# Performance work log

Hardware: AMD Instinct MI355X
Metric: run time of the kernel (lower is better)

Reference implementation:

```python
import jax, jax.numpy as jnp
import numpy as np

B, N, D, H = 4, 4096, 1024, 16
DH = D // H            # 64
GH = 4 * DH            # gate hidden = 256
FREQ = N // 2 + 1      # 2049
INV_SQRT2 = 0.7071067811865476


def _ln(x, g, b, eps=1e-6):
    mu = jnp.mean(x, axis=-1, keepdims=True)
    var = jnp.mean((x - mu) ** 2, axis=-1, keepdims=True)
    return (x - mu) / jnp.sqrt(var + eps) * g + b


def _xavier(k, out_f, in_f, gain=0.8):
    bound = gain * (6.0 / (in_f + out_f)) ** 0.5
    return jax.random.uniform(k, (out_f, in_f), jnp.float32, -bound, bound)


def setup_inputs() -> dict:
    key = jax.random.key(0)
    ks = jax.random.split(key, 8)
    return {
        'x': jax.random.normal(ks[0], (B, N, D), jnp.float32),
        'Wq': _xavier(ks[1], D, D),
        'Wv': _xavier(ks[2], D, D),
        'Wo': _xavier(ks[3], D, D),
        'ln_g': jnp.ones((DH,), jnp.float32),
        'ln_b': jnp.zeros((DH,), jnp.float32),
        'Wgup': _xavier(ks[4], GH, DH),
        'Wgdn': _xavier(ks[5], 2 * FREQ, GH),
        'Wwup': _xavier(ks[6], GH, DH),
        'Wwdn': _xavier(ks[7], N, GH),
    }


def reference(x, Wq, Wv, Wo, ln_g, ln_b, Wgup, Wgdn, Wwup, Wwdn):
    Bx, Nx, Dx = x.shape
    # projections -> [B, H, N, DH]
    q = (x @ Wq.T).reshape(Bx, Nx, H, DH).transpose(0, 2, 1, 3)
    v = (x @ Wv.T).reshape(Bx, Nx, H, DH).transpose(0, 2, 1, 3)
    # per-head summary token -> complex spectral gate over FREQ bins
    bar = _ln(q.mean(axis=2), ln_g, ln_b)                    # [B, H, DH]
    gr = (jax.nn.silu(bar @ Wgup.T) @ Wgdn.T)               # [B, H, 2*FREQ]
    gr = gr.reshape(Bx, H, FREQ, 2)
    gate = jax.lax.complex(gr[..., 0], gr[..., 1])           # [B, H, FREQ]
    # spectral mixing (chunk == seq_len, power-of-two path)
    spec = jnp.fft.rfft(v, axis=2, norm='ortho') * gate[..., None]
    v_t = jnp.fft.irfft(spec, n=Nx, axis=2, norm='ortho')    # [B, H, N, DH]
    # Haar wavelet refinement
    even, odd = v_t[..., ::2, :], v_t[..., 1::2, :]
    w = jnp.concatenate([even + odd, even - odd], axis=-2) * INV_SQRT2
    s = (jax.nn.silu(bar @ Wwup.T) @ Wwdn.T)[..., None]      # [B, H, N, 1]
    w = w * s
    half = Nx // 2
    low, high = w[..., :half, :], w[..., half:, :]
    # interleave even/odd back along seq dim
    refine = jnp.stack([low + high, low - high], axis=-2).reshape(Bx, H, Nx, DH) * INV_SQRT2
    v_t = v_t + refine
    y = v_t.transpose(0, 2, 1, 3).reshape(Bx, Nx, Dx)
    return y @ Wo.T
```

## Files before the change

### kernel.cpp

```cpp
#include <hip/hip_runtime.h>

constexpr int CB = 4, CN = 4096, CD = 1024, CH = 16, CDH = 64, CGH = 256, CFREQ = 2049, CBH = 64;

constexpr size_t OFF_XSUM = 0;
constexpr size_t OFF_HG   = 4096;
constexpr size_t OFF_HW   = OFF_HG + (size_t)CBH * CGH;
constexpr size_t OFF_GATE = OFF_HW + (size_t)CBH * CGH;
constexpr size_t OFF_S    = OFF_GATE + (size_t)CBH * 2 * CFREQ;
constexpr size_t OFF_CA   = OFF_S + (size_t)CBH * CN;
constexpr size_t OFF_CD   = OFF_CA + (size_t)CBH * (CN / 2);
constexpr size_t OFF_TW   = OFF_CD + (size_t)CBH * (CN / 2);
constexpr size_t OFF_VCOL = OFF_TW + 8192;
constexpr size_t OFF_XHI  = OFF_VCOL + (size_t)CB * CD * CN;
constexpr size_t OFF_XLO  = OFF_XHI + (size_t)CB * CN * CD / 2;
constexpr size_t OFF_WVHI = OFF_XLO + (size_t)CB * CN * CD / 2;
constexpr size_t OFF_WVLO = OFF_WVHI + (size_t)CD * CD / 2;
constexpr size_t OFF_WOHI = OFF_WVLO + (size_t)CD * CD / 2;
constexpr size_t OFF_WOLO = OFF_WOHI + (size_t)CD * CD / 2;

typedef __bf16 bf16x8 __attribute__((ext_vector_type(8)));
typedef __bf16 bf16x4 __attribute__((ext_vector_type(4)));
typedef float  f32x4  __attribute__((ext_vector_type(4)));

__device__ __forceinline__ float silu_f(float x) { return x / (1.0f + expf(-x)); }

__device__ __forceinline__ void gload16(const void* g, void* l) {
    __builtin_amdgcn_global_load_lds(
        reinterpret_cast<const __attribute__((address_space(1))) unsigned int*>(
            reinterpret_cast<uintptr_t>(g)),
        reinterpret_cast<__attribute__((address_space(3))) unsigned int*>(
            reinterpret_cast<uintptr_t>(l)),
        16, 0, 0);
}

__device__ __forceinline__ float2 cadd(float2 a, float2 b) { return make_float2(a.x + b.x, a.y + b.y); }
__device__ __forceinline__ float2 csub(float2 a, float2 b) { return make_float2(a.x - b.x, a.y - b.y); }
__device__ __forceinline__ float2 cmul(float2 a, float2 b) { return make_float2(a.x * b.x - a.y * b.y, a.x * b.y + a.y * b.x); }
__device__ __forceinline__ float2 cmulc(float2 a, float2 b) { return make_float2(a.x * b.x + a.y * b.y, a.y * b.x - a.x * b.y); }
__device__ __forceinline__ float2 mulni(float2 a) { return make_float2(a.y, -a.x); }
__device__ __forceinline__ float2 mulpi(float2 a) { return make_float2(-a.y, a.x); }

__device__ __forceinline__ int P(int r) { return r + (r >> 3); }

__device__ __forceinline__ int drev8(int k) {
    return ((k & 7) << 9) | (((k >> 3) & 7) << 6) | (((k >> 6) & 7) << 3) | ((k >> 9) & 7);
}

__device__ __forceinline__ void dft8_fwd(const float2 a[8], float2 A[8]) {
    float2 t0 = cadd(a[0], a[4]), t1 = csub(a[0], a[4]);
    float2 t2 = cadd(a[2], a[6]), t3 = mulni(csub(a[2], a[6]));
    float2 t4 = cadd(a[1], a[5]), t5 = csub(a[1], a[5]);
    float2 t6 = cadd(a[3], a[7]), t7 = mulni(csub(a[3], a[7]));
    float2 u0 = cadd(t0, t2), u1 = csub(t0, t2);
    float2 u2 = cadd(t1, t3), u3 = csub(t1, t3);
    float2 u4 = cadd(t4, t6), u5 = mulni(csub(t4, t6));
    float2 u6 = cadd(t5, t7), u7 = csub(t5, t7);
    const float s = 0.70710678118654752f;
    float2 w6 = make_float2(s * (u6.x + u6.y), s * (u6.y - u6.x));
    float2 w7 = make_float2(s * (u7.y - u7.x), -s * (u7.x + u7.y));
    A[0] = cadd(u0, u4); A[4] = csub(u0, u4);
    A[2] = cadd(u1, u5); A[6] = csub(u1, u5);
    A[1] = cadd(u2, w6); A[5] = csub(u2, w6);
    A[3] = cadd(u3, w7); A[7] = csub(u3, w7);
}

__device__ __forceinline__ void dft8_inv(const float2 a[8], float2 A[8]) {
    float2 t0 = cadd(a[0], a[4]), t1 = csub(a[0], a[4]);
    float2 t2 = cadd(a[2], a[6]), t3 = mulpi(csub(a[2], a[6]));
    float2 t4 = cadd(a[1], a[5]), t5 = csub(a[1], a[5]);
    float2 t6 = cadd(a[3], a[7]), t7 = mulpi(csub(a[3], a[7]));
    float2 u0 = cadd(t0, t2), u1 = csub(t0, t2);
    float2 u2 = cadd(t1, t3), u3 = csub(t1, t3);
    float2 u4 = cadd(t4, t6), u5 = mulpi(csub(t4, t6));
    float2 u6 = cadd(t5, t7), u7 = csub(t5, t7);
    const float s = 0.70710678118654752f;
    float2 w6 = make_float2(s * (u6.x - u6.y), s * (u6.x + u6.y));
    float2 w7 = make_float2(-s * (u7.x + u7.y), s * (u7.x - u7.y));
    A[0] = cadd(u0, u4); A[4] = csub(u0, u4);
    A[2] = cadd(u1, u5); A[6] = csub(u1, u5);
    A[1] = cadd(u2, w6); A[5] = csub(u2, w6);
    A[3] = cadd(u3, w7); A[7] = csub(u3, w7);
}

template <int M>
__device__ __forceinline__ void fwd_stage(float2* buf, const float2* __restrict__ tw, int t) {
    int j = t & (M - 1);
    int i0 = ((t & ~(M - 1)) << 3) + j;
    constexpr int TS = 512 / M;
    float2 a[8], A[8];
#pragma unroll
    for (int c = 0; c < 8; ++c) a[c] = buf[P(i0 + c * M)];
    dft8_fwd(a, A);
#pragma unroll
    for (int p = 0; p < 8; ++p) {
        float2 v = (M > 1 && p) ? cmul(A[p], tw[j * p * TS]) : A[p];
        buf[P(i0 + p * M)] = v;
    }
}

template <int M>
__device__ __forceinline__ void inv_stage(float2* buf, const float2* __restrict__ tw, int t) {
    int j = t & (M - 1);
    int i0 = ((t & ~(M - 1)) << 3) + j;
    constexpr int TS = 512 / M;
    float2 a[8], A[8];
#pragma unroll
    for (int c = 0; c < 8; ++c) {
        float2 v = buf[P(i0 + c * M)];
        a[c] = (M > 1 && c) ? cmulc(v, tw[j * c * TS]) : v;
    }
    dft8_inv(a, A);
#pragma unroll
    for (int p = 0; p < 8; ++p) buf[P(i0 + p * M)] = A[p];
}

__global__ void k_tw(float* twf) {
    int i = blockIdx.x * 256 + threadIdx.x;
    if (i < 4096) {
        double ang = -2.0 * 3.14159265358979323846 * (double)i / 4096.0;
        twf[2 * i]     = (float)cos(ang);
        twf[2 * i + 1] = (float)sin(ang);
    }
}

__global__ __launch_bounds__(256) void k_meansplit(const float* __restrict__ X, float* __restrict__ xsum,
                                                   __bf16* __restrict__ hi, __bf16* __restrict__ lo) {
    int b = blockIdx.y;
    int c = blockIdx.x;
    int t = threadIdx.x;
    int half = t >> 7;
    int col = (t & 127) * 8;
    size_t base = (size_t)b * CN * CD + ((size_t)c * 64 + half * 32) * CD + col;
    float acc[8];
#pragma unroll
    for (int j = 0; j < 8; ++j) acc[j] = 0.f;
    for (int n = 0; n < 32; ++n) {
        size_t o = base + (size_t)n * CD;
        float4 v0 = *(const float4*)(X + o);
        float4 v1 = *(const float4*)(X + o + 4);
        float vv[8] = {v0.x, v0.y, v0.z, v0.w, v1.x, v1.y, v1.z, v1.w};
        bf16x8 hv, lv;
#pragma unroll
        for (int j = 0; j < 8; ++j) {
            acc[j] += vv[j];
            __bf16 h = (__bf16)vv[j];
            hv[j] = h;
            lv[j] = (__bf16)(vv[j] - (float)h);
        }
        *(bf16x8*)&hi[o] = hv;
        *(bf16x8*)&lo[o] = lv;
    }
#pragma unroll
    for (int j = 0; j < 8; ++j) atomicAdd(&xsum[b * CD + col + j], acc[j]);
}

__global__ __launch_bounds__(256) void k_barhidden(const float* __restrict__ xsum,
                                                   const float* __restrict__ Wq,
                                                   const float* __restrict__ ln_g,
                                                   const float* __restrict__ ln_b,
                                                   const float* __restrict__ Wgup,
                                                   const float* __restrict__ Wwup,
                                                   float* __restrict__ hg, float* __restrict__ hw) {
    int bh = blockIdx.x;
    int b = bh >> 4, h = bh & 15;
    int t = threadIdx.x;
    __shared__ float part[256];
    __shared__ float bar_s[64];
    int dh = t >> 2, seg = t & 3;
    const float* wrow = Wq + (size_t)(h * 64 + dh) * CD + seg * 256;
    const float* xs = xsum + b * CD + seg * 256;
    float acc = 0.f;
    for (int i = 0; i < 256; i += 4) {
        float4 w4 = *(const float4*)(wrow + i);
        float4 x4 = *(const float4*)(xs + i);
        acc += w4.x * x4.x + w4.y * x4.y + w4.z * x4.z + w4.w * x4.w;
    }
    part[t] = acc;
    __syncthreads();
    if (t < 64) {
        float q = (part[4 * t] + part[4 * t + 1] + part[4 * t + 2] + part[4 * t + 3]) * (1.0f / 4096.0f);
        float mu = q;
        for (int o = 32; o >= 1; o >>= 1) mu += __shfl_xor(mu, o, 64);
        mu *= (1.0f / 64.0f);
        float dev = q - mu;
        float vv = dev * dev;
        for (int o = 32; o >= 1; o >>= 1) vv += __shfl_xor(vv, o, 64);
        vv *= (1.0f / 64.0f);
        bar_s[t] = dev / sqrtf(vv + 1e-6f) * ln_g[t] + ln_b[t];
    }
    __syncthreads();
    const float* gup = Wgup + (size_t)t * CDH;
    const float* wup = Wwup + (size_t)t * CDH;
    float ag = 0.f, aw = 0.f;
    for (int i = 0; i < CDH; i += 4) {
        float4 bb = *(const float4*)(&bar_s[i]);
        float4 g4 = *(const float4*)(gup + i);
        float4 w4 = *(const float4*)(wup + i);
        ag += g4.x * bb.x + g4.y * bb.y + g4.z * bb.z + g4.w * bb.w;
        aw += w4.x * bb.x + w4.y * bb.y + w4.z * bb.z + w4.w * bb.w;
    }
    hg[bh * CGH + t] = silu_f(ag);
    hw[bh * CGH + t] = silu_f(aw);
}

__global__ __launch_bounds__(256) void k_gategemv(const float* __restrict__ Wgdn,
                                                  const float* __restrict__ Wwdn,
                                                  const float* __restrict__ hg,
                                                  const float* __restrict__ hw,
                                                  float* __restrict__ gate, float* __restrict__ sbuf) {
    int z = blockIdx.z;
    const float* Wd = z ? Wwdn : Wgdn;
    const float* hid = z ? hw : hg;
    float* out = z ? sbuf : gate;
    int Kout = z ? CN : 2 * CFREQ;
    int bh0 = blockIdx.y * 8;
    int t = threadIdx.x;
    int k = blockIdx.x * 256 + t;
    __shared__ float Lh[8][256];
    for (int g = 0; g < 8; ++g) Lh[g][t] = hid[(size_t)(bh0 + g) * CGH + t];
    __syncthreads();
    if (k >= Kout) return;
    float accv[8] = {0.f, 0.f, 0.f, 0.f, 0.f, 0.f, 0.f, 0.f};
    const float* wrow = Wd + (size_t)k * CGH;
    for (int j4 = 0; j4 < 64; ++j4) {
        float4 wv = *(const float4*)(wrow + 4 * j4);
#pragma unroll
        for (int g = 0; g < 8; ++g) {
            accv[g] += wv.x * Lh[g][4 * j4] + wv.y * Lh[g][4 * j4 + 1] +
                       wv.z * Lh[g][4 * j4 + 2] + wv.w * Lh[g][4 * j4 + 3];
        }
    }
    for (int g = 0; g < 8; ++g) out[(size_t)(bh0 + g) * Kout + k] = accv[g];
}

__global__ __launch_bounds__(256) void k_coef(const float* __restrict__ sbuf,
                                              float* __restrict__ ca, float* __restrict__ cd) {
    int bh = blockIdx.y;
    int i = blockIdx.x * 256 + threadIdx.x;
    float s0 = sbuf[(size_t)bh * CN + i];
    float s1 = sbuf[(size_t)bh * CN + 2048 + i];
    ca[(size_t)bh * 2048 + i] = 1.0f + 0.5f * (s0 + s1);
    cd[(size_t)bh * 2048 + i] = 0.5f * (s0 - s1);
}

__global__ __launch_bounds__(256) void k_split(const float* __restrict__ src,
                                               __bf16* __restrict__ hi, __bf16* __restrict__ lo,
                                               int n4) {
    int i = blockIdx.x * 256 + threadIdx.x;
    int stride = gridDim.x * 256;
    for (; i < n4; i += stride) {
        float4 v = ((const float4*)src)[i];
        __bf16 h0 = (__bf16)v.x, h1 = (__bf16)v.y, h2 = (__bf16)v.z, h3 = (__bf16)v.w;
        bf16x4 hv = {h0, h1, h2, h3};
        bf16x4 lv = {(__bf16)(v.x - (float)h0), (__bf16)(v.y - (float)h1),
                     (__bf16)(v.z - (float)h2), (__bf16)(v.w - (float)h3)};
        *(bf16x4*)&hi[4 * (size_t)i] = hv;
        *(bf16x4*)&lo[4 * (size_t)i] = lv;
    }
}

__global__ __launch_bounds__(256) void k_tsplit(const float* __restrict__ Vcol,
                                                __bf16* __restrict__ hi, __bf16* __restrict__ lo) {
    __shared__ float tile[32][33];
    int bx = blockIdx.x;
    int by = blockIdx.y;
    int b  = blockIdx.z;
    int t = threadIdx.x;
    int d = t >> 3, n4 = (t & 7) * 4;
    const float* src = Vcol + ((size_t)b * CD + by * 32 + d) * CN + bx * 32 + n4;
    float4 v = *(const float4*)src;
    tile[d][n4] = v.x; tile[d][n4 + 1] = v.y; tile[d][n4 + 2] = v.z; tile[d][n4 + 3] = v.w;
    __syncthreads();
    int n = t >> 3, d4 = (t & 7) * 4;
    size_t o = ((size_t)b * CN + bx * 32 + n) * CD + by * 32 + d4;
    float x0 = tile[d4][n], x1 = tile[d4 + 1][n], x2 = tile[d4 + 2][n], x3 = tile[d4 + 3][n];
    __bf16 h0 = (__bf16)x0, h1 = (__bf16)x1, h2 = (__bf16)x2, h3 = (__bf16)x3;
    bf16x4 hv = {h0, h1, h2, h3};
    bf16x4 lv = {(__bf16)(x0 - (float)h0), (__bf16)(x1 - (float)h1),
                 (__bf16)(x2 - (float)h2), (__bf16)(x3 - (float)h3)};
    *(bf16x4*)&hi[o] = hv;
    *(bf16x4*)&lo[o] = lv;
}

template <int TRANS>
__global__ __launch_bounds__(256) void k_mfma_gemm(const __bf16* __restrict__ Ahi,
                                                   const __bf16* __restrict__ Alo,
                                                   const __bf16* __restrict__ Bhi,
                                                   const __bf16* __restrict__ Blo,
                                                   float* __restrict__ C) {
    __shared__ __align__(16) __bf16 lds[2][4][128 * 32];
    int t = threadIdx.x;
    int l = t & 63, w = t >> 6;
    int hw = blockIdx.x + (blockIdx.y << 3);
    int xcd = hw & 7, slot = hw >> 3;
    int m0 = (xcd * 16 + (slot >> 3)) * 128;
    int n0 = (slot & 7) * 128;
    int wm = w >> 1, wn = w & 1;

    const __bf16* gsrc = (w == 0) ? Ahi : (w == 1) ? Alo : (w == 2) ? Bhi : Blo;
    int gr0 = (w < 2) ? m0 : n0;
    unsigned o[8];
#pragma unroll
    for (int i = 0; i < 8; ++i) {
        int row = i * 16 + (l >> 2);
        unsigned slotq = (unsigned)((l & 3) ^ ((row >> 2) & 3));
        o[i] = (unsigned)(gr0 + row) * 1024u + slotq * 8u;
    }

    f32x4 acc[4][4];
#pragma unroll
    for (int m = 0; m < 4; ++m)
#pragma unroll
        for (int n = 0; n < 4; ++n) acc[m][n] = (f32x4){0.f, 0.f, 0.f, 0.f};

#pragma unroll
    for (int i = 0; i < 8; ++i)
        gload16(gsrc + (size_t)o[i], &lds[0][w][i * 512]);
    __syncthreads();

    int cur = 0;
#pragma unroll 2
    for (int k0 = 0; k0 < 1024; k0 += 32) {
        if (k0 + 32 < 1024) {
#pragma unroll
            for (int i = 0; i < 8; ++i)
                gload16(gsrc + ((size_t)o[i] + k0 + 32), &lds[cur ^ 1][w][i * 512]);
        }

        bf16x8 ah[4], al[4], bh[4], bl[4];
#pragma unroll
        for (int m = 0; m < 4; ++m) {
            int row = wm * 64 + m * 16 + (l & 15);
            int sl = (l >> 4) ^ ((row >> 2) & 3);
            ah[m] = *(const bf16x8*)&lds[cur][0][row * 32 + sl * 8];
            al[m] = *(const bf16x8*)&lds[cur][1][row * 32 + sl * 8];
        }
#pragma unroll
        for (int n = 0; n < 4; ++n) {
            int row = wn * 64 + n * 16 + (l & 15);
            int sl = (l >> 4) ^ ((row >> 2) & 3);
            bh[n] = *(const bf16x8*)&lds[cur][2][row * 32 + sl * 8];
            bl[n] = *(const bf16x8*)&lds[cur][3][row * 32 + sl * 8];
        }
#pragma unroll
        for (int m = 0; m < 4; ++m)
#pragma unroll
            for (int n = 0; n < 4; ++n) {
                acc[m][n] = __builtin_amdgcn_mfma_f32_16x16x32_bf16(ah[m], bh[n], acc[m][n], 0, 0, 0);
                acc[m][n] = __builtin_amdgcn_mfma_f32_16x16x32_bf16(ah[m], bl[n], acc[m][n], 0, 0, 0);
                acc[m][n] = __builtin_amdgcn_mfma_f32_16x16x32_bf16(al[m], bh[n], acc[m][n], 0, 0, 0);
            }
        __syncthreads();
        cur ^= 1;
    }

    if (TRANS) {
        int b = m0 >> 12;
        int tokb = (m0 & 4095) + wm * 64;
#pragma unroll
        for (int m = 0; m < 4; ++m)
#pragma unroll
            for (int n = 0; n < 4; ++n) {
                int dcol = n0 + wn * 64 + n * 16 + (l & 15);
                int tok = tokb + m * 16 + ((l >> 4) << 2);
                *(f32x4*)&C[((size_t)(b * CD + dcol)) * CN + tok] = acc[m][n];
            }
    } else {
#pragma unroll
        for (int m = 0; m < 4; ++m)
#pragma unroll
            for (int n = 0; n < 4; ++n) {
                int r0 = m0 + wm * 64 + m * 16 + ((l >> 4) << 2);
                int cc = n0 + wn * 64 + n * 16 + (l & 15);
#pragma unroll
                for (int q = 0; q < 4; ++q) C[(size_t)(r0 + q) * CD + cc] = acc[m][n][q];
            }
    }
}

__global__ __launch_bounds__(512) void k_fft(float* __restrict__ Vcol,
                                             const float* __restrict__ gateB,
                                             const float* __restrict__ caB,
                                             const float* __restrict__ cdB,
                                             const float2* __restrict__ tw) {
    __shared__ float2 buf[4608];
    int blk = blockIdx.x;
    int bh = blk >> 5, pr = blk & 31;
    int t = threadIdx.x;
    float* colA = Vcol + (size_t)(bh * 64 + pr * 2) * CN;
    float* colB = colA + CN;

    {
        float2 a[8], A[8];
#pragma unroll
        for (int c = 0; c < 8; ++c) {
            int n = t + 512 * c;
            a[c] = make_float2(colA[n], colB[n]);
        }
        dft8_fwd(a, A);
#pragma unroll
        for (int p = 0; p < 8; ++p) {
            float2 v = p ? cmul(A[p], tw[t * p]) : A[p];
            buf[P(t + 512 * p)] = v;
        }
    }
    __syncthreads();
    fwd_stage<64>(buf, tw, t);  __syncthreads();
    fwd_stage<8>(buf, tw, t);   __syncthreads();
    fwd_stage<1>(buf, tw, t);   __syncthreads();

    {
        const float2* g2 = (const float2*)gateB + (size_t)bh * CFREQ;
        for (int k = t; k <= 2048; k += 512) {
            int r  = drev8(k);
            int r2 = drev8((4096 - k) & 4095);
            float2 Zk = buf[P(r)];
            float2 Zj = buf[P(r2)];
            float2 Av = make_float2(0.5f * (Zk.x + Zj.x), 0.5f * (Zk.y - Zj.y));
            float2 Bv = make_float2(0.5f * (Zk.y + Zj.y), -0.5f * (Zk.x - Zj.x));
            float2 g = g2[k];
            float2 SA = cmul(g, Av);
            float2 SB = cmul(g, Bv);
            buf[P(r)] = make_float2(SA.x - SB.y, SA.y + SB.x);
            if (r2 != r) buf[P(r2)] = make_float2(SA.x + SB.y, SB.x - SA.y);
        }
    }
    __syncthreads();

    inv_stage<1>(buf, tw, t);   __syncthreads();
    inv_stage<8>(buf, tw, t);   __syncthreads();
    inv_stage<64>(buf, tw, t);  __syncthreads();

    {
        float2 a[8], A[8];
#pragma unroll
        for (int c = 0; c < 8; ++c) {
            float2 v = buf[P(t + 512 * c)];
            a[c] = c ? cmulc(v, tw[t * c]) : v;
        }
        dft8_inv(a, A);
        const float scale = 1.0f / 4096.0f;
        const float* ca = caB + (size_t)bh * 2048;
        const float* cd = cdB + (size_t)bh * 2048;
#pragma unroll
        for (int p = 0; p < 8; ++p) {
            int n = t + 512 * p;
            int i = n >> 1;
            float A_ = ca[i] * scale, D_ = cd[i] * scale;
            float ox = __shfl_xor(A[p].x, 1, 64);
            float oy = __shfl_xor(A[p].y, 1, 64);
            colA[n] = A_ * A[p].x + D_ * ox;
            colB[n] = A_ * A[p].y + D_ * oy;
        }
    }
}

extern "C" void kernel_launch(void* const* d_in, const int* in_sizes, int n_in,
                              void* d_out, int out_size, void* d_ws, size_t ws_size,
                              hipStream_t stream) {
    const float* x    = (const float*)d_in[0];
    const float* Wq   = (const float*)d_in[1];
    const float* Wv   = (const float*)d_in[2];
    const float* Wo   = (const float*)d_in[3];
    const float* ln_g = (const float*)d_in[4];
    const float* ln_b = (const float*)d_in[5];
    const float* Wgup = (const float*)d_in[6];
    const float* Wgdn = (const float*)d_in[7];
    const float* Wwup = (const float*)d_in[8];
    const float* Wwdn = (const float*)d_in[9];
    float* ws  = (float*)d_ws;
    float* out = (float*)d_out;

    __bf16* xhi  = (__bf16*)(ws + OFF_XHI);
    __bf16* xlo  = (__bf16*)(ws + OFF_XLO);
    __bf16* wvhi = (__bf16*)(ws + OFF_WVHI);
    __bf16* wvlo = (__bf16*)(ws + OFF_WVLO);
    __bf16* wohi = (__bf16*)(ws + OFF_WOHI);
    __bf16* wolo = (__bf16*)(ws + OFF_WOLO);
    __bf16* v2hi = (__bf16*)(ws + OFF_XHI);
    __bf16* v2lo = (__bf16*)(ws + OFF_XLO);

    hipMemsetAsync(ws + OFF_XSUM, 0, 4096 * sizeof(float), stream);
    k_tw<<<16, 256, 0, stream>>>(ws + OFF_TW);
    k_meansplit<<<dim3(64, 4), 256, 0, stream>>>(x, ws + OFF_XSUM, xhi, xlo);
    k_barhidden<<<64, 256, 0, stream>>>(ws + OFF_XSUM, Wq, ln_g, ln_b, Wgup, Wwup,
                                        ws + OFF_HG, ws + OFF_HW);
    k_gategemv<<<dim3(17, 8, 2), 256, 0, stream>>>(Wgdn, Wwdn, ws + OFF_HG, ws + OFF_HW,
                                                   ws + OFF_GATE, ws + OFF_S);
    k_coef<<<dim3(8, 64), 256, 0, stream>>>(ws + OFF_S, ws + OFF_CA, ws + OFF_CD);

    k_split<<<1024, 256, 0, stream>>>(Wv, wvhi, wvlo, CD * CD / 4);
    k_split<<<1024, 256, 0, stream>>>(Wo, wohi, wolo, CD * CD / 4);

    k_mfma_gemm<1><<<dim3(8, 128), 256, 0, stream>>>(xhi, xlo, wvhi, wvlo, ws + OFF_VCOL);

    k_fft<<<2048, 512, 0, stream>>>(ws + OFF_VCOL, ws + OFF_GATE, ws + OFF_CA, ws + OFF_CD,
                                    (const float2*)(ws + OFF_TW));

    k_tsplit<<<dim3(128, 32, 4), 256, 0, stream>>>(ws + OFF_VCOL, v2hi, v2lo);

    k_mfma_gemm<0><<<dim3(8, 128), 256, 0, stream>>>(v2hi, v2lo, wohi, wolo, out);
}
```

Baseline: 416.7 us.

## Retile split-bf16 GEMM to 256x256 blocks with 32x32 MFMA and interleaved prefetch

Enlarges the GEMM block tile from 128x128 to 256x256 with 512 threads and switches to 32x32x16 MFMA instructions, each wave computing a 128x64 sub-tile. Global-to-LDS prefetch of the next K slice is interleaved with the MFMA phases, which are bracketed by barriers and setprio. This aims to raise operand reuse and MFMA efficiency, at the cost of 128 KB of LDS per block, a single block per CU, and higher register pressure.

```diff
diff --git a/kernel.cpp b/kernel.cpp
--- a/kernel.cpp
+++ b/kernel.cpp
@@ -21,6 +21,7 @@
 typedef __bf16 bf16x8 __attribute__((ext_vector_type(8)));
 typedef __bf16 bf16x4 __attribute__((ext_vector_type(4)));
 typedef float  f32x4  __attribute__((ext_vector_type(4)));
+typedef float  f32x16 __attribute__((ext_vector_type(16)));
 
 __device__ __forceinline__ float silu_f(float x) { return x / (1.0f + expf(-x)); }
 
@@ -283,97 +284,126 @@
 }
 
 template <int TRANS>
-__global__ __launch_bounds__(256) void k_mfma_gemm(const __bf16* __restrict__ Ahi,
-                                                   const __bf16* __restrict__ Alo,
-                                                   const __bf16* __restrict__ Bhi,
-                                                   const __bf16* __restrict__ Blo,
-                                                   float* __restrict__ C) {
-    __shared__ __align__(16) __bf16 lds[2][4][128 * 32];
+__global__ __launch_bounds__(512, 2) void k_mfma_gemm(const __bf16* __restrict__ Ahi,
+                                                      const __bf16* __restrict__ Alo,
+                                                      const __bf16* __restrict__ Bhi,
+                                                      const __bf16* __restrict__ Blo,
+                                                      float* __restrict__ C) {
+    __shared__ __align__(16) __bf16 lds[2][4][256 * 32];
     int t = threadIdx.x;
     int l = t & 63, w = t >> 6;
-    int hw = blockIdx.x + (blockIdx.y << 3);
+    int wm = w >> 2, wn = w & 3;
+    int hw = blockIdx.x;
     int xcd = hw & 7, slot = hw >> 3;
-    int m0 = (xcd * 16 + (slot >> 3)) * 128;
-    int n0 = (slot & 7) * 128;
-    int wm = w >> 1, wn = w & 1;
-
-    const __bf16* gsrc = (w == 0) ? Ahi : (w == 1) ? Alo : (w == 2) ? Bhi : Blo;
-    int gr0 = (w < 2) ? m0 : n0;
+    int m0 = (xcd * 8 + (slot >> 2)) * 256;
+    int n0 = (slot & 3) * 256;
+
+    int pl = w >> 1;
+    const __bf16* gsrc = (pl == 0) ? Ahi : (pl == 1) ? Alo : (pl == 2) ? Bhi : Blo;
+    int gr0 = (pl < 2) ? m0 : n0;
     unsigned o[8];
+    int rl0[8];
 #pragma unroll
     for (int i = 0; i < 8; ++i) {
-        int row = i * 16 + (l >> 2);
-        unsigned slotq = (unsigned)((l & 3) ^ ((row >> 2) & 3));
-        o[i] = (unsigned)(gr0 + row) * 1024u + slotq * 8u;
-    }
-
-    f32x4 acc[4][4];
-#pragma unroll
-    for (int m = 0; m < 4; ++m)
-#pragma unroll
-        for (int n = 0; n < 4; ++n) acc[m][n] = (f32x4){0.f, 0.f, 0.f, 0.f};
+        int rl = (w & 1) * 128 + i * 16 + (l >> 2);
+        unsigned sq = (unsigned)((l & 3) ^ ((rl >> 2) & 3));
+        o[i] = (unsigned)(gr0 + rl) * 1024u + sq * 8u;
+        rl0[i] = (w & 1) * 128 + i * 16;
+    }
+
+    f32x16 acc[4][2];
+#pragma unroll
+    for (int mi = 0; mi < 4; ++mi)
+#pragma unroll
+        for (int ni = 0; ni < 2; ++ni)
+#pragma unroll
+            for (int q = 0; q < 16; ++q) acc[mi][ni][q] = 0.f;
 
 #pragma unroll
     for (int i = 0; i < 8; ++i)
-        gload16(gsrc + (size_t)o[i], &lds[0][w][i * 512]);
-    __syncthreads();
-
-    int cur = 0;
-#pragma unroll 2
-    for (int k0 = 0; k0 < 1024; k0 += 32) {
-        if (k0 + 32 < 1024) {
-#pragma unroll
-            for (int i = 0; i < 8; ++i)
-                gload16(gsrc + ((size_t)o[i] + k0 + 32), &lds[cur ^ 1][w][i * 512]);
-        }
-
-        bf16x8 ah[4], al[4], bh[4], bl[4];
-#pragma unroll
-        for (int m = 0; m < 4; ++m) {
-            int row = wm * 64 + m * 16 + (l & 15);
-            int sl = (l >> 4) ^ ((row >> 2) & 3);
-            ah[m] = *(const bf16x8*)&lds[cur][0][row * 32 + sl * 8];
-            al[m] = *(const bf16x8*)&lds[cur][1][row * 32 + sl * 8];
-        }
-#pragma unroll
-        for (int n = 0; n < 4; ++n) {
-            int row = wn * 64 + n * 16 + (l & 15);
-            int sl = (l >> 4) ^ ((row >> 2) & 3);
-            bh[n] = *(const bf16x8*)&lds[cur][2][row * 32 + sl * 8];
-            bl[n] = *(const bf16x8*)&lds[cur][3][row * 32 + sl * 8];
-        }
-#pragma unroll
-        for (int m = 0; m < 4; ++m)
-#pragma unroll
-            for (int n = 0; n < 4; ++n) {
-                acc[m][n] = __builtin_amdgcn_mfma_f32_16x16x32_bf16(ah[m], bh[n], acc[m][n], 0, 0, 0);
-                acc[m][n] = __builtin_amdgcn_mfma_f32_16x16x32_bf16(ah[m], bl[n], acc[m][n], 0, 0, 0);
-                acc[m][n] = __builtin_amdgcn_mfma_f32_16x16x32_bf16(al[m], bh[n], acc[m][n], 0, 0, 0);
+        gload16(gsrc + (size_t)o[i], &lds[0][pl][rl0[i] * 32]);
+    __syncthreads();
+
+#pragma unroll 1
+    for (int t32 = 0; t32 < 32; ++t32) {
+        int cur = t32 & 1;
+        size_t koff = (size_t)(t32 + 1) * 32;
+        bool pf = (t32 + 1) < 32;
+        bf16x8 bfr[2][2][2];
+#pragma unroll
+        for (int p = 0; p < 4; ++p) {
+            if (pf) {
+                gload16(gsrc + ((size_t)o[2 * p] + koff), &lds[cur ^ 1][pl][rl0[2 * p] * 32]);
+                gload16(gsrc + ((size_t)o[2 * p + 1] + koff), &lds[cur ^ 1][pl][rl0[2 * p + 1] * 32]);
             }
+            bf16x8 afr[2][2];
+            int arow = wm * 128 + p * 32 + (l & 31);
+            int akey = (arow >> 2) & 3;
+#pragma unroll
+            for (int s = 0; s < 2; ++s) {
+                int sl = ((l >> 5) + 2 * s) ^ akey;
+                afr[s][0] = *(const bf16x8*)&lds[cur][0][arow * 32 + sl * 8];
+                afr[s][1] = *(const bf16x8*)&lds[cur][1][arow * 32 + sl * 8];
+            }
+            if (p == 0) {
+#pragma unroll
+                for (int ni = 0; ni < 2; ++ni) {
+                    int bcol = wn * 64 + ni * 32 + (l & 31);
+                    int bkey = (bcol >> 2) & 3;
+#pragma unroll
+                    for (int s = 0; s < 2; ++s) {
+                        int sl = ((l >> 5) + 2 * s) ^ bkey;
+                        bfr[ni][s][0] = *(const bf16x8*)&lds[cur][2][bcol * 32 + sl * 8];
+                        bfr[ni][s][1] = *(const bf16x8*)&lds[cur][3][bcol * 32 + sl * 8];
+                    }
+                }
+            }
+            __builtin_amdgcn_s_barrier();
+            __builtin_amdgcn_s_setprio(1);
+#pragma unroll
+            for (int ni = 0; ni < 2; ++ni)
+#pragma unroll
+                for (int s = 0; s < 2; ++s) {
+                    acc[p][ni] = __builtin_amdgcn_mfma_f32_32x32x16_bf16(afr[s][0], bfr[ni][s][0], acc[p][ni], 0, 0, 0);
+                    acc[p][ni] = __builtin_amdgcn_mfma_f32_32x32x16_bf16(afr[s][0], bfr[ni][s][1], acc[p][ni], 0, 0, 0);
+                    acc[p][ni] = __builtin_amdgcn_mfma_f32_32x32x16_bf16(afr[s][1], bfr[ni][s][0], acc[p][ni], 0, 0, 0);
+                }
+            __builtin_amdgcn_s_setprio(0);
+            __builtin_amdgcn_s_barrier();
+        }
         __syncthreads();
-        cur ^= 1;
     }
 
     if (TRANS) {
         int b = m0 >> 12;
-        int tokb = (m0 & 4095) + wm * 64;
-#pragma unroll
-        for (int m = 0; m < 4; ++m)
-#pragma unroll
-            for (int n = 0; n < 4; ++n) {
-                int dcol = n0 + wn * 64 + n * 16 + (l & 15);
-                int tok = tokb + m * 16 + ((l >> 4) << 2);
-                *(f32x4*)&C[((size_t)(b * CD + dcol)) * CN + tok] = acc[m][n];
+        int tokb = (m0 & 4095) + wm * 128;
+#pragma unroll
+        for (int mi = 0; mi < 4; ++mi)
+#pragma unroll
+            for (int ni = 0; ni < 2; ++ni) {
+                int dcol = n0 + wn * 64 + ni * 32 + (l & 31);
+                float* base = C + ((size_t)(b * CD + dcol)) * CN;
+#pragma unroll
+                for (int q = 0; q < 4; ++q) {
+                    int tok = tokb + mi * 32 + 8 * q + 4 * (l >> 5);
+                    f32x4 v = {acc[mi][ni][4 * q], acc[mi][ni][4 * q + 1],
+                               acc[mi][ni][4 * q + 2], acc[mi][ni][4 * q + 3]};
+                    *(f32x4*)&base[tok] = v;
+                }
             }
     } else {
 #pragma unroll
-        for (int m = 0; m < 4; ++m)
-#pragma unroll
-            for (int n = 0; n < 4; ++n) {
-                int r0 = m0 + wm * 64 + m * 16 + ((l >> 4) << 2);
-                int cc = n0 + wn * 64 + n * 16 + (l & 15);
-#pragma unroll
-                for (int q = 0; q < 4; ++q) C[(size_t)(r0 + q) * CD + cc] = acc[m][n][q];
+        for (int mi = 0; mi < 4; ++mi)
+#pragma unroll
+            for (int ni = 0; ni < 2; ++ni) {
+                int cc = n0 + wn * 64 + ni * 32 + (l & 31);
+#pragma unroll
+                for (int q = 0; q < 4; ++q) {
+                    int r0 = m0 + wm * 128 + mi * 32 + 8 * q + 4 * (l >> 5);
+#pragma unroll
+                    for (int j = 0; j < 4; ++j)
+                        C[(size_t)(r0 + j) * CD + cc] = acc[mi][ni][4 * q + j];
+                }
             }
     }
 }
@@ -492,12 +522,12 @@
     k_split<<<1024, 256, 0, stream>>>(Wv, wvhi, wvlo, CD * CD / 4);
     k_split<<<1024, 256, 0, stream>>>(Wo, wohi, wolo, CD * CD / 4);
 
-    k_mfma_gemm<1><<<dim3(8, 128), 256, 0, stream>>>(xhi, xlo, wvhi, wvlo, ws + OFF_VCOL);
+    k_mfma_gemm<1><<<256, 512, 0, stream>>>(xhi, xlo, wvhi, wvlo, ws + OFF_VCOL);
 
     k_fft<<<2048, 512, 0, stream>>>(ws + OFF_VCOL, ws + OFF_GATE, ws + OFF_CA, ws + OFF_CD,
                                     (const float2*)(ws + OFF_TW));
 
     k_tsplit<<<dim3(128, 32, 4), 256, 0, stream>>>(ws + OFF_VCOL, v2hi, v2lo);
 
-    k_mfma_gemm<0><<<dim3(8, 128), 256, 0, stream>>>(v2hi, v2lo, wohi, wolo, out);
-}
+    k_mfma_gemm<0><<<256, 512, 0, stream>>>(v2hi, v2lo, wohi, wolo, out);
+}
```

Measured after the change: 403.3 us. 3.2% less time.
